# Performance work log

Hardware: AMD Instinct MI355X
Metric: run time of the kernel (lower is better)

The kernel has to match this reference:

```python
import jax, jax.numpy as jnp
import numpy as np

HEADS = 16


def setup_inputs() -> dict:
    key = jax.random.key(0)
    k1, k2, k3 = jax.random.split(key, 3)
    B, T, D = 2, 2048, 1024
    x = jax.random.normal(k1, (B, T, D), dtype=jnp.float32)
    # causal mask, broadcast over batch and heads
    mask = jnp.tril(jnp.ones((T, T), dtype=bool))[None, None, :, :]
    # torch Linear(dim, 3*dim, bias=False): weight [3D, D]; we store transposed [D, 3D]
    Wqkv = jax.random.normal(k2, (D, 3 * D), dtype=jnp.float32) * (D ** -0.5)
    Wo = jax.random.normal(k3, (D, D), dtype=jnp.float32) * (D ** -0.5)
    return {"x": x, "mask": mask, "Wqkv": Wqkv, "Wo": Wo}


def reference(x, mask, Wqkv, Wo):
    B, T, D = x.shape
    h = HEADS
    dh = D // h
    scale = dh ** -0.5
    qkv = (x @ Wqkv).reshape(B, T, 3, h, dh)
    qkv = jnp.transpose(qkv, (2, 0, 3, 1, 4))  # [3, B, h, T, dh]
    q, k, v = qkv[0], qkv[1], qkv[2]
    att = jnp.einsum("bhqd,bhkd->bhqk", q, k) * scale  # [B, h, T, T]
    att = jnp.where(mask, att, jnp.float32(-1e9))
    att = jax.nn.softmax(att, axis=-1)
    # dropout: identity in eval/reference mode
    out = jnp.einsum("bhqk,bhkd->bhqd", att, v)  # [B, h, T, dh]
    out = jnp.transpose(out, (0, 2, 1, 3)).reshape(B, T, D)
    return out @ Wo
```

## Files before the change

kernel.cpp:

```cpp
#include <hip/hip_runtime.h>
#include <cstdint>

typedef unsigned short ushort_t;
typedef __attribute__((ext_vector_type(8))) short short8;
typedef __attribute__((ext_vector_type(4))) float f32x4;

#define B_ 2
#define T_ 2048
#define D_ 1024
#define H_ 16
#define DH_ 64

__device__ inline unsigned short f2bf(float f) {
  unsigned int u = __float_as_uint(f);
  u += 0x7FFF + ((u >> 16) & 1);
  return (unsigned short)(u >> 16);
}

__device__ inline unsigned short f2bf_fast(float f) {
  return (unsigned short)((__float_as_uint(f) + 0x8000u) >> 16);
}

__device__ inline f32x4 mfma16(short8 a, short8 b, f32x4 c) {
  return __builtin_amdgcn_mfma_f32_16x16x32_bf16(a, b, c, 0, 0, 0);
}

__device__ inline void gload16(const void* g, void* l) {
  __builtin_amdgcn_global_load_lds(
      (const __attribute__((address_space(1))) unsigned int*)(uintptr_t)g,
      (__attribute__((address_space(3))) unsigned int*)(uint32_t)(uintptr_t)l,
      16, 0, 0);
}

__global__ void k_cvt(const float* __restrict__ in, ushort_t* __restrict__ out, int n4) {
  int i = blockIdx.x * blockDim.x + threadIdx.x;
  if (i >= n4) return;
  float4 v = ((const float4*)in)[i];
  ushort4 o;
  o.x = f2bf(v.x); o.y = f2bf(v.y); o.z = f2bf(v.z); o.w = f2bf(v.w);
  ((ushort4*)out)[i] = o;
}

__global__ void k_tcvt(const float* __restrict__ in, ushort_t* __restrict__ out,
                       int R, int C) {
  __shared__ float tile[32][33];
  int c0 = blockIdx.x * 32, r0 = blockIdx.y * 32;
  int tx = threadIdx.x, ty = threadIdx.y;
#pragma unroll
  for (int i = 0; i < 32; i += 8)
    tile[ty + i][tx] = in[(size_t)(r0 + ty + i) * C + c0 + tx];
  __syncthreads();
#pragma unroll
  for (int i = 0; i < 32; i += 8)
    out[(size_t)(c0 + ty + i) * R + r0 + tx] = f2bf(tile[tx][ty + i]);
}

__global__ __launch_bounds__(256, 2) void k_gemm_qkv(
    const ushort_t* __restrict__ A, const ushort_t* __restrict__ Bt,
    ushort_t* __restrict__ pq, ushort_t* __restrict__ pk,
    ushort_t* __restrict__ pv) {
  const int K = 1024, Kb = 2 * K;
  __shared__ __align__(16) ushort_t As[128 * 32];
  __shared__ __align__(16) ushort_t Bs[128 * 32];
  const int tid = threadIdx.x;
  const int w = tid >> 6, l = tid & 63;
  const int bm = blockIdx.y, bn = blockIdx.x;
  const int wm = w >> 1, wn = w & 1;

  const f32x4 fz = {0.f, 0.f, 0.f, 0.f};
  f32x4 acc[4][4];
#pragma unroll
  for (int i = 0; i < 4; ++i)
#pragma unroll
    for (int j = 0; j < 4; ++j) acc[i][j] = fz;

  const int r_a = l >> 2;
  const int cb = (l & 3) * 16;
  const int lrow = l & 15;
  const int lk16 = (l >> 4) * 16;

  for (int k0 = 0; k0 < K; k0 += 32) {
    __syncthreads();
#pragma unroll
    for (int c = 0; c < 2; ++c) {
      int row = (w * 2 + c) * 16 + r_a;
      gload16((const char*)A + (size_t)(bm * 128 + row) * Kb + k0 * 2 + cb,
              (char*)As + row * 64 + cb);
      gload16((const char*)Bt + (size_t)(bn * 128 + row) * Kb + k0 * 2 + cb,
              (char*)Bs + row * 64 + cb);
    }
    __syncthreads();
    short8 af[4], bv[4];
#pragma unroll
    for (int mt = 0; mt < 4; ++mt)
      af[mt] = *(const short8*)((const char*)As + (wm * 64 + mt * 16 + lrow) * 64 + lk16);
#pragma unroll
    for (int nt = 0; nt < 4; ++nt)
      bv[nt] = *(const short8*)((const char*)Bs + (wn * 64 + nt * 16 + lrow) * 64 + lk16);
#pragma unroll
    for (int mt = 0; mt < 4; ++mt)
#pragma unroll
      for (int nt = 0; nt < 4; ++nt)
        acc[mt][nt] = mfma16(af[mt], bv[nt], acc[mt][nt]);
  }

  const int rg = (l >> 4) * 4;
  const int s = bn >> 3;
  const float QS = 0.125f * 1.44269504f;
#pragma unroll
  for (int mt = 0; mt < 4; ++mt)
#pragma unroll
    for (int nt = 0; nt < 4; ++nt) {
      int gcol = bn * 128 + wn * 64 + nt * 16 + lrow;
      int dh = gcol & 63, hh = (gcol >> 6) & 15;
#pragma unroll
      for (int r = 0; r < 4; ++r) {
        int grow = bm * 128 + wm * 64 + mt * 16 + rg + r;
        int b = grow >> 11, trow = grow & 2047;
        int bh = b * 16 + hh;
        float v = acc[mt][nt][r];
        if (s == 0) v *= QS;
        unsigned short u = f2bf(v);
        if (s < 2) {
          ushort_t* base = s ? pk : pq;
          size_t off = (size_t)bh * (128 * 1024) + (size_t)(trow >> 4) * 1024 +
                       (size_t)(dh >> 5) * 512 +
                       (((trow & 15) + ((dh >> 3) & 3) * 16) << 3) + (dh & 7);
          base[off] = (ushort_t)u;
        } else {
          size_t off = ((size_t)(bh * 64 + (trow >> 5)) * 4 + (dh >> 4)) * 512 +
                       (((dh & 15) + ((trow >> 3) & 3) * 16) << 3) + (trow & 7);
          pv[off] = (ushort_t)u;
        }
      }
    }
}

template <int OUTF>
__global__ __launch_bounds__(256, 2) void k_gemm_bt(
    const ushort_t* __restrict__ A, const ushort_t* __restrict__ Bt,
    void* __restrict__ C, int M, int N, int K) {
  __shared__ __align__(16) ushort_t As[128 * 32];
  __shared__ __align__(16) ushort_t Bs[128 * 32];
  const int tid = threadIdx.x;
  const int w = tid >> 6, l = tid & 63;
  const int bm = blockIdx.y, bn = blockIdx.x;
  const int wm = w >> 1, wn = w & 1;

  const f32x4 fz = {0.f, 0.f, 0.f, 0.f};
  f32x4 acc[4][4];
#pragma unroll
  for (int i = 0; i < 4; ++i)
#pragma unroll
    for (int j = 0; j < 4; ++j) acc[i][j] = fz;

  const int r_a = l >> 2;
  const int cb = (l & 3) * 16;
  const int lrow = l & 15;
  const int lk16 = (l >> 4) * 16;

  for (int k0 = 0; k0 < K; k0 += 32) {
    __syncthreads();
#pragma unroll
    for (int c = 0; c < 2; ++c) {
      int row = (w * 2 + c) * 16 + r_a;
      gload16((const char*)A + ((size_t)(bm * 128 + row) * K + k0) * 2 + cb,
              (char*)As + row * 64 + cb);
      gload16((const char*)Bt + ((size_t)(bn * 128 + row) * K + k0) * 2 + cb,
              (char*)Bs + row * 64 + cb);
    }
    __syncthreads();
    short8 af[4], bv[4];
#pragma unroll
    for (int mt = 0; mt < 4; ++mt)
      af[mt] = *(const short8*)((const char*)As + (wm * 64 + mt * 16 + lrow) * 64 + lk16);
#pragma unroll
    for (int nt = 0; nt < 4; ++nt)
      bv[nt] = *(const short8*)((const char*)Bs + (wn * 64 + nt * 16 + lrow) * 64 + lk16);
#pragma unroll
    for (int mt = 0; mt < 4; ++mt)
#pragma unroll
      for (int nt = 0; nt < 4; ++nt)
        acc[mt][nt] = mfma16(af[mt], bv[nt], acc[mt][nt]);
  }

  const int rg = (l >> 4) * 4;
#pragma unroll
  for (int mt = 0; mt < 4; ++mt)
#pragma unroll
    for (int nt = 0; nt < 4; ++nt) {
      size_t col = (size_t)bn * 128 + wn * 64 + nt * 16 + lrow;
#pragma unroll
      for (int r = 0; r < 4; ++r) {
        size_t rowi = (size_t)bm * 128 + wm * 64 + mt * 16 + rg + r;
        if (OUTF)
          ((float*)C)[rowi * N + col] = acc[mt][nt][r];
        else
          ((ushort_t*)C)[rowi * N + col] = f2bf(acc[mt][nt][r]);
      }
    }
}

__global__ __launch_bounds__(64) void k_attn(
    const ushort_t* __restrict__ pq, const ushort_t* __restrict__ pk,
    const ushort_t* __restrict__ pv, ushort_t* __restrict__ ctx) {
  __shared__ __align__(16) ushort_t plds[2][16][72];
  const int l = threadIdx.x;
  const int n = blockIdx.x;
  const int q = n >> 3;
  const int bh = (n & 7) * 4 + (q & 3);
  const int j2 = 63 - (q >> 2);
  const int b = bh >> 4, hh = bh & 15;
  const int jlo = j2 * 2;
  const int qr0 = jlo * 16;
  const int lrow = l & 15, lg = l >> 4;

  const ushort_t* pqb = pq + (size_t)(bh * 128 + jlo) * 1024 + l * 8;
  short8 aq00 = *(const short8*)(pqb);
  short8 aq01 = *(const short8*)(pqb + 512);
  short8 aq10 = *(const short8*)(pqb + 1024);
  short8 aq11 = *(const short8*)(pqb + 1536);

  const f32x4 fz = {0.f, 0.f, 0.f, 0.f};
  f32x4 o0[4], o1[4];
#pragma unroll
  for (int nt = 0; nt < 4; ++nt) { o0[nt] = fz; o1[nt] = fz; }
  float ls0[4] = {0.f, 0.f, 0.f, 0.f};
  float ls1[4] = {0.f, 0.f, 0.f, 0.f};

  const int ntiles = (j2 >> 1) + 1;
  for (int t = 0; t < ntiles; ++t) {
    const int kv0 = t * 64;
    const ushort_t* pkb = pk + (size_t)(bh * 128 + (kv0 >> 4)) * 1024 + l * 8;
    short8 bk0[4], bk1[4];
#pragma unroll
    for (int nh = 0; nh < 4; ++nh) {
      bk0[nh] = *(const short8*)(pkb + nh * 1024);
      bk1[nh] = *(const short8*)(pkb + nh * 1024 + 512);
    }
    f32x4 s0[4], s1[4];
    __builtin_amdgcn_s_setprio(1);
#pragma unroll
    for (int nh = 0; nh < 4; ++nh) {
      s0[nh] = mfma16(aq01, bk1[nh], mfma16(aq00, bk0[nh], fz));
      s1[nh] = mfma16(aq11, bk1[nh], mfma16(aq10, bk0[nh], fz));
    }
    __builtin_amdgcn_s_setprio(0);
    if (t == ntiles - 1) {
#pragma unroll
      for (int r = 0; r < 4; ++r) {
        int row0 = qr0 + lg * 4 + r;
#pragma unroll
        for (int nh = 0; nh < 4; ++nh) {
          int col = kv0 + nh * 16 + lrow;
          if (col > row0)      s0[nh][r] = -1e30f;
          if (col > row0 + 16) s1[nh][r] = -1e30f;
        }
      }
    }
    const ushort_t* pvb = pv + (size_t)(bh * 64 + (kv0 >> 5)) * 2048 + l * 8;
    short8 bv0[4], bv1[4];
#pragma unroll
    for (int nt = 0; nt < 4; ++nt) {
      bv0[nt] = *(const short8*)(pvb + nt * 512);
      bv1[nt] = *(const short8*)(pvb + 2048 + nt * 512);
    }
#pragma unroll
    for (int r = 0; r < 4; ++r) {
      float a0 = __builtin_amdgcn_exp2f(s0[0][r]);
      float a1 = __builtin_amdgcn_exp2f(s0[1][r]);
      float a2 = __builtin_amdgcn_exp2f(s0[2][r]);
      float a3 = __builtin_amdgcn_exp2f(s0[3][r]);
      float c0 = __builtin_amdgcn_exp2f(s1[0][r]);
      float c1 = __builtin_amdgcn_exp2f(s1[1][r]);
      float c2 = __builtin_amdgcn_exp2f(s1[2][r]);
      float c3 = __builtin_amdgcn_exp2f(s1[3][r]);
      ls0[r] += (a0 + a1) + (a2 + a3);
      ls1[r] += (c0 + c1) + (c2 + c3);
      plds[0][lg * 4 + r][lrow]      = f2bf_fast(a0);
      plds[0][lg * 4 + r][16 + lrow] = f2bf_fast(a1);
      plds[0][lg * 4 + r][32 + lrow] = f2bf_fast(a2);
      plds[0][lg * 4 + r][48 + lrow] = f2bf_fast(a3);
      plds[1][lg * 4 + r][lrow]      = f2bf_fast(c0);
      plds[1][lg * 4 + r][16 + lrow] = f2bf_fast(c1);
      plds[1][lg * 4 + r][32 + lrow] = f2bf_fast(c2);
      plds[1][lg * 4 + r][48 + lrow] = f2bf_fast(c3);
    }
    short8 pa00 = *(const short8*)&plds[0][lrow][lg * 8];
    short8 pa01 = *(const short8*)&plds[0][lrow][32 + lg * 8];
    short8 pa10 = *(const short8*)&plds[1][lrow][lg * 8];
    short8 pa11 = *(const short8*)&plds[1][lrow][32 + lg * 8];
    __builtin_amdgcn_s_setprio(1);
#pragma unroll
    for (int nt = 0; nt < 4; ++nt) {
      o0[nt] = mfma16(pa01, bv1[nt], mfma16(pa00, bv0[nt], o0[nt]));
      o1[nt] = mfma16(pa11, bv1[nt], mfma16(pa10, bv0[nt], o1[nt]));
    }
    __builtin_amdgcn_s_setprio(0);
  }
#pragma unroll
  for (int r = 0; r < 4; ++r) {
#pragma unroll
    for (int x = 1; x < 16; x <<= 1) {
      ls0[r] += __shfl_xor(ls0[r], x);
      ls1[r] += __shfl_xor(ls1[r], x);
    }
  }
#pragma unroll
  for (int nt = 0; nt < 4; ++nt) {
#pragma unroll
    for (int r = 0; r < 4; ++r) {
      int row0 = qr0 + lg * 4 + r;
      size_t base = (size_t)b * T_ + row0;
      ctx[(base) * D_ + hh * DH_ + nt * 16 + lrow] =
          f2bf(o0[nt][r] / ls0[r]);
      ctx[(base + 16) * D_ + hh * DH_ + nt * 16 + lrow] =
          f2bf(o1[nt][r] / ls1[r]);
    }
  }
}

extern "C" void kernel_launch(void* const* d_in, const int* in_sizes, int n_in,
                              void* d_out, int out_size, void* d_ws, size_t ws_size,
                              hipStream_t stream) {
  const float* x    = (const float*)d_in[0];
  const float* Wqkv = (const float*)d_in[2];
  const float* Wo   = (const float*)d_in[3];
  float* out = (float*)d_out;

  char* ws = (char*)d_ws;
  ushort_t* xb    = (ushort_t*)(ws);
  ushort_t* wqkvT = (ushort_t*)(ws + (8u  << 20));
  ushort_t* woT   = (ushort_t*)(ws + (14u << 20));
  ushort_t* pq    = (ushort_t*)(ws + (16u << 20));
  ushort_t* pk    = (ushort_t*)(ws + (24u << 20));
  ushort_t* pv    = (ushort_t*)(ws + (32u << 20));
  ushort_t* ctxb  = (ushort_t*)(ws + (40u << 20));

  dim3 tb(32, 8);
  k_cvt<<<(B_ * T_ * D_) / 4 / 256, 256, 0, stream>>>(x, xb, (B_ * T_ * D_) / 4);
  k_tcvt<<<dim3(96, 32), tb, 0, stream>>>(Wqkv, wqkvT, 1024, 3072);
  k_tcvt<<<dim3(32, 32), tb, 0, stream>>>(Wo, woT, 1024, 1024);
  k_gemm_qkv<<<dim3(24, 32), 256, 0, stream>>>(xb, wqkvT, pq, pk, pv);
  k_attn<<<2048, 64, 0, stream>>>(pq, pk, pv, ctxb);
  k_gemm_bt<1><<<dim3(8, 32), 256, 0, stream>>>(ctxb, woT, out, 4096, 1024, 1024);
}
```

Measured before the change: 195.7 us.

## Stage QKV epilogue through LDS for vector stores; double-buffer K/V loads in attention

The QKV GEMM epilogue now writes the packed tile into shared memory in the swizzled Q/K/V layouts and then copies it out with coalesced 16-byte stores. This replaces scattered 2-byte global writes. The attention loop is software-pipelined with two register sets, so the next tile's K and V fragments are loaded while the current tile is computed. This adds register pressure and one extra LDS round-trip and barrier in the GEMM epilogue.

```diff
diff --git a/kernel.cpp b/kernel.cpp
--- a/kernel.cpp
+++ b/kernel.cpp
@@ -60,8 +60,9 @@
     ushort_t* __restrict__ pq, ushort_t* __restrict__ pk,
     ushort_t* __restrict__ pv) {
   const int K = 1024, Kb = 2 * K;
-  __shared__ __align__(16) ushort_t As[128 * 32];
-  __shared__ __align__(16) ushort_t Bs[128 * 32];
+  __shared__ __align__(16) ushort_t smem[16384];
+  ushort_t* As = smem;
+  ushort_t* Bs = smem + 4096;
   const int tid = threadIdx.x;
   const int w = tid >> 6, l = tid & 63;
   const int bm = blockIdx.y, bn = blockIdx.x;
@@ -103,37 +104,56 @@
       for (int nt = 0; nt < 4; ++nt)
         acc[mt][nt] = mfma16(af[mt], bv[nt], acc[mt][nt]);
   }
+  __syncthreads();
 
   const int rg = (l >> 4) * 4;
   const int s = bn >> 3;
+  const int bns = bn & 7;
+  const int bb = bm >> 4;
   const float QS = 0.125f * 1.44269504f;
+
 #pragma unroll
   for (int mt = 0; mt < 4; ++mt)
 #pragma unroll
     for (int nt = 0; nt < 4; ++nt) {
-      int gcol = bn * 128 + wn * 64 + nt * 16 + lrow;
-      int dh = gcol & 63, hh = (gcol >> 6) & 15;
+      int gc = wn * 64 + nt * 16 + lrow;
+      int hsel = gc >> 6, dh = gc & 63;
 #pragma unroll
       for (int r = 0; r < 4; ++r) {
-        int grow = bm * 128 + wm * 64 + mt * 16 + rg + r;
-        int b = grow >> 11, trow = grow & 2047;
-        int bh = b * 16 + hh;
+        int gl = wm * 64 + mt * 16 + rg + r;
         float v = acc[mt][nt][r];
         if (s == 0) v *= QS;
         unsigned short u = f2bf(v);
-        if (s < 2) {
-          ushort_t* base = s ? pk : pq;
-          size_t off = (size_t)bh * (128 * 1024) + (size_t)(trow >> 4) * 1024 +
-                       (size_t)(dh >> 5) * 512 +
-                       (((trow & 15) + ((dh >> 3) & 3) * 16) << 3) + (dh & 7);
-          base[off] = (ushort_t)u;
-        } else {
-          size_t off = ((size_t)(bh * 64 + (trow >> 5)) * 4 + (dh >> 4)) * 512 +
-                       (((dh & 15) + ((trow >> 3) & 3) * 16) << 3) + (trow & 7);
-          pv[off] = (ushort_t)u;
-        }
+        int idx;
+        if (s < 2)
+          idx = (((hsel << 4) + ((gl >> 4) << 1) + (dh >> 5)) << 9) +
+                (((gl & 15) + ((dh >> 3) & 3) * 16) << 3) + (dh & 7);
+        else
+          idx = (((hsel << 4) + ((gl >> 5) << 2) + (dh >> 4)) << 9) +
+                (((dh & 15) + ((gl >> 3) & 3) * 16) << 3) + (gl & 7);
+        smem[idx] = (ushort_t)u;
       }
     }
+  __syncthreads();
+
+  ushort_t* dstT = (s == 0) ? pq : (s == 1 ? pk : pv);
+#pragma unroll
+  for (int it = 0; it < 8; ++it) {
+    int j = it * 256 + tid;
+    int lane = j & 63, chunk = j >> 6;
+    int hsel = chunk >> 4;
+    int bhs = bb * 16 + bns * 2 + hsel;
+    size_t off;
+    if (s < 2) {
+      int t16l = (chunk >> 1) & 7, half = chunk & 1;
+      off = (size_t)bhs * (128 * 1024) +
+            (size_t)((bm & 15) * 8 + t16l) * 1024 + half * 512 + lane * 8;
+    } else {
+      int t32l = (chunk >> 2) & 3, ntv = chunk & 3;
+      off = ((size_t)(bhs * 64 + (bm & 15) * 4 + t32l) * 4 + ntv) * 512 + lane * 8;
+    }
+    *(short8*)(dstT + off) = *(const short8*)(smem + j * 8);
+  }
 }
 
 template <int OUTF>
@@ -229,75 +249,88 @@
   float ls1[4] = {0.f, 0.f, 0.f, 0.f};
 
   const int ntiles = (j2 >> 1) + 1;
-  for (int t = 0; t < ntiles; ++t) {
-    const int kv0 = t * 64;
-    const ushort_t* pkb = pk + (size_t)(bh * 128 + (kv0 >> 4)) * 1024 + l * 8;
-    short8 bk0[4], bk1[4];
-#pragma unroll
-    for (int nh = 0; nh < 4; ++nh) {
-      bk0[nh] = *(const short8*)(pkb + nh * 1024);
-      bk1[nh] = *(const short8*)(pkb + nh * 1024 + 512);
-    }
-    f32x4 s0[4], s1[4];
-    __builtin_amdgcn_s_setprio(1);
-#pragma unroll
-    for (int nh = 0; nh < 4; ++nh) {
-      s0[nh] = mfma16(aq01, bk1[nh], mfma16(aq00, bk0[nh], fz));
-      s1[nh] = mfma16(aq11, bk1[nh], mfma16(aq10, bk0[nh], fz));
-    }
-    __builtin_amdgcn_s_setprio(0);
-    if (t == ntiles - 1) {
-#pragma unroll
-      for (int r = 0; r < 4; ++r) {
-        int row0 = qr0 + lg * 4 + r;
-#pragma unroll
-        for (int nh = 0; nh < 4; ++nh) {
-          int col = kv0 + nh * 16 + lrow;
-          if (col > row0)      s0[nh][r] = -1e30f;
-          if (col > row0 + 16) s1[nh][r] = -1e30f;
-        }
-      }
-    }
-    const ushort_t* pvb = pv + (size_t)(bh * 64 + (kv0 >> 5)) * 2048 + l * 8;
-    short8 bv0[4], bv1[4];
-#pragma unroll
-    for (int nt = 0; nt < 4; ++nt) {
-      bv0[nt] = *(const short8*)(pvb + nt * 512);
-      bv1[nt] = *(const short8*)(pvb + 2048 + nt * 512);
-    }
-#pragma unroll
-    for (int r = 0; r < 4; ++r) {
-      float a0 = __builtin_amdgcn_exp2f(s0[0][r]);
-      float a1 = __builtin_amdgcn_exp2f(s0[1][r]);
-      float a2 = __builtin_amdgcn_exp2f(s0[2][r]);
-      float a3 = __builtin_amdgcn_exp2f(s0[3][r]);
-      float c0 = __builtin_amdgcn_exp2f(s1[0][r]);
-      float c1 = __builtin_amdgcn_exp2f(s1[1][r]);
-      float c2 = __builtin_amdgcn_exp2f(s1[2][r]);
-      float c3 = __builtin_amdgcn_exp2f(s1[3][r]);
-      ls0[r] += (a0 + a1) + (a2 + a3);
-      ls1[r] += (c0 + c1) + (c2 + c3);
-      plds[0][lg * 4 + r][lrow]      = f2bf_fast(a0);
-      plds[0][lg * 4 + r][16 + lrow] = f2bf_fast(a1);
-      plds[0][lg * 4 + r][32 + lrow] = f2bf_fast(a2);
-      plds[0][lg * 4 + r][48 + lrow] = f2bf_fast(a3);
-      plds[1][lg * 4 + r][lrow]      = f2bf_fast(c0);
-      plds[1][lg * 4 + r][16 + lrow] = f2bf_fast(c1);
-      plds[1][lg * 4 + r][32 + lrow] = f2bf_fast(c2);
-      plds[1][lg * 4 + r][48 + lrow] = f2bf_fast(c3);
-    }
-    short8 pa00 = *(const short8*)&plds[0][lrow][lg * 8];
-    short8 pa01 = *(const short8*)&plds[0][lrow][32 + lg * 8];
-    short8 pa10 = *(const short8*)&plds[1][lrow][lg * 8];
-    short8 pa11 = *(const short8*)&plds[1][lrow][32 + lg * 8];
-    __builtin_amdgcn_s_setprio(1);
-#pragma unroll
-    for (int nt = 0; nt < 4; ++nt) {
-      o0[nt] = mfma16(pa01, bv1[nt], mfma16(pa00, bv0[nt], o0[nt]));
-      o1[nt] = mfma16(pa11, bv1[nt], mfma16(pa10, bv0[nt], o1[nt]));
-    }
-    __builtin_amdgcn_s_setprio(0);
-  }
+
+  short8 Ka0[4], Ka1[4], Va0[4], Va1[4];
+  short8 Kb0[4], Kb1[4], Vb0[4], Vb1[4];
+
+#define LOADKV(K0, K1, V0, V1, tt)                                          \
+  {                                                                         \
+    const ushort_t* pkb_ = pk + (size_t)(bh * 128 + ((tt) << 2)) * 1024 + l * 8; \
+    _Pragma("unroll") for (int nh = 0; nh < 4; ++nh) {                      \
+      K0[nh] = *(const short8*)(pkb_ + nh * 1024);                          \
+      K1[nh] = *(const short8*)(pkb_ + nh * 1024 + 512);                    \
+    }                                                                       \
+    const ushort_t* pvb_ = pv + (size_t)(bh * 64 + ((tt) << 1)) * 2048 + l * 8; \
+    _Pragma("unroll") for (int nt = 0; nt < 4; ++nt) {                      \
+      V0[nt] = *(const short8*)(pvb_ + nt * 512);                           \
+      V1[nt] = *(const short8*)(pvb_ + 2048 + nt * 512);                    \
+    }                                                                       \
+  }
+
+#define COMPUTE(tt, K0, K1, V0, V1)                                         \
+  {                                                                         \
+    f32x4 s0[4], s1[4];                                                     \
+    __builtin_amdgcn_s_setprio(1);                                          \
+    _Pragma("unroll") for (int nh = 0; nh < 4; ++nh) {                      \
+      s0[nh] = mfma16(aq01, K1[nh], mfma16(aq00, K0[nh], fz));              \
+      s1[nh] = mfma16(aq11, K1[nh], mfma16(aq10, K0[nh], fz));              \
+    }                                                                       \
+    __builtin_amdgcn_s_setprio(0);                                          \
+    if ((tt) == ntiles - 1) {                                               \
+      _Pragma("unroll") for (int r = 0; r < 4; ++r) {                       \
+        int row0 = qr0 + lg * 4 + r;                                        \
+        _Pragma("unroll") for (int nh = 0; nh < 4; ++nh) {                  \
+          int col = (tt) * 64 + nh * 16 + lrow;                             \
+          if (col > row0)      s0[nh][r] = -1e30f;                          \
+          if (col > row0 + 16) s1[nh][r] = -1e30f;                          \
+        }                                                                   \
+      }                                                                     \
+    }                                                                       \
+    _Pragma("unroll") for (int r = 0; r < 4; ++r) {                         \
+      float a0 = __builtin_amdgcn_exp2f(s0[0][r]);                          \
+      float a1 = __builtin_amdgcn_exp2f(s0[1][r]);                          \
+      float a2 = __builtin_amdgcn_exp2f(s0[2][r]);                          \
+      float a3 = __builtin_amdgcn_exp2f(s0[3][r]);                          \
+      float c0 = __builtin_amdgcn_exp2f(s1[0][r]);                          \
+      float c1 = __builtin_amdgcn_exp2f(s1[1][r]);                          \
+      float c2 = __builtin_amdgcn_exp2f(s1[2][r]);                          \
+      float c3 = __builtin_amdgcn_exp2f(s1[3][r]);                          \
+      ls0[r] += (a0 + a1) + (a2 + a3);                                      \
+      ls1[r] += (c0 + c1) + (c2 + c3);                                      \
+      plds[0][lg * 4 + r][lrow]      = f2bf_fast(a0);                       \
+      plds[0][lg * 4 + r][16 + lrow] = f2bf_fast(a1);                       \
+      plds[0][lg * 4 + r][32 + lrow] = f2bf_fast(a2);                       \
+      plds[0][lg * 4 + r][48 + lrow] = f2bf_fast(a3);                       \
+      plds[1][lg * 4 + r][lrow]      = f2bf_fast(c0);                       \
+      plds[1][lg * 4 + r][16 + lrow] = f2bf_fast(c1);                       \
+      plds[1][lg * 4 + r][32 + lrow] = f2bf_fast(c2);                       \
+      plds[1][lg * 4 + r][48 + lrow] = f2bf_fast(c3);                       \
+    }                                                                       \
+    short8 pa00 = *(const short8*)&plds[0][lrow][lg * 8];                   \
+    short8 pa01 = *(const short8*)&plds[0][lrow][32 + lg * 8];              \
+    short8 pa10 = *(const short8*)&plds[1][lrow][lg * 8];                   \
+    short8 pa11 = *(const short8*)&plds[1][lrow][32 + lg * 8];              \
+    __builtin_amdgcn_s_setprio(1);                                          \
+    _Pragma("unroll") for (int nt = 0; nt < 4; ++nt) {                      \
+      o0[nt] = mfma16(pa01, V1[nt], mfma16(pa00, V0[nt], o0[nt]));          \
+      o1[nt] = mfma16(pa11, V1[nt], mfma16(pa10, V0[nt], o1[nt]));          \
+    }                                                                       \
+    __builtin_amdgcn_s_setprio(0);                                          \
+  }
+
+  LOADKV(Ka0, Ka1, Va0, Va1, 0);
+  int t = 0;
+  while (true) {
+    if (t + 1 < ntiles) LOADKV(Kb0, Kb1, Vb0, Vb1, t + 1);
+    COMPUTE(t, Ka0, Ka1, Va0, Va1);
+    if (++t >= ntiles) break;
+    if (t + 1 < ntiles) LOADKV(Ka0, Ka1, Va0, Va1, t + 1);
+    COMPUTE(t, Kb0, Kb1, Vb0, Vb1);
+    if (++t >= ntiles) break;
+  }
+#undef LOADKV
+#undef COMPUTE
+
 #pragma unroll
   for (int r = 0; r < 4; ++r) {
 #pragma unroll
```

Result: no change. 192.8 us (-1.5%).
